# Performance work log

Measured on AMD Instinct MI355X. Metric: run time of the kernel, lower is better.

## Reference

```python
import jax, jax.numpy as jnp
import numpy as np

B, N, K, IN_CH = 512, 64, 16, 6   # graphs, nodes per graph, knn, input features
EPS = 1e-5


def _w(key, shape, fan_in):
    return jax.random.normal(key, shape, jnp.float32) / np.sqrt(fan_in)


def setup_inputs() -> dict:
    key = jax.random.key(0)
    ks = jax.random.split(key, 16)
    f32 = jnp.float32
    inp = {
        "x": jax.random.normal(ks[0], (B * N, IN_CH), f32),
        "batch": (jnp.arange(B * N, dtype=jnp.int32) // N).astype(jnp.int32),
        # input projection 6 -> 64
        "w_in": _w(ks[1], (IN_CH, 64), IN_CH), "g_in": jnp.ones(64, f32), "b_in": jnp.zeros(64, f32),
        # ec1: SharedMLP([128, 64, 64])
        "w1a": _w(ks[2], (128, 64), 128), "g1a": jnp.ones(64, f32), "b1a": jnp.zeros(64, f32),
        "w1b": _w(ks[3], (64, 64), 64),   "g1b": jnp.ones(64, f32), "b1b": jnp.zeros(64, f32),
        # ec2: SharedMLP([128, 128, 128])
        "w2a": _w(ks[4], (128, 128), 128), "g2a": jnp.ones(128, f32), "b2a": jnp.zeros(128, f32),
        "w2b": _w(ks[5], (128, 128), 128), "g2b": jnp.ones(128, f32), "b2b": jnp.zeros(128, f32),
        # ec3: SharedMLP([256, 256, 256])
        "w3a": _w(ks[6], (256, 256), 256), "g3a": jnp.ones(256, f32), "b3a": jnp.zeros(256, f32),
        "w3b": _w(ks[7], (256, 256), 256), "g3b": jnp.ones(256, f32), "b3b": jnp.zeros(256, f32),
        # classifier head (dropout is identity in eval mode)
        "wc1": _w(ks[8], (896, 512), 896), "gc1": jnp.ones(512, f32), "bc1": jnp.zeros(512, f32),
        "wc2": _w(ks[9], (512, 256), 512), "gc2": jnp.ones(256, f32), "bc2": jnp.zeros(256, f32),
        "wc3": _w(ks[10], (256, 2), 256),  "bc3": jnp.zeros(2, f32),
    }
    return inp


def bn(h, g, b):
    # training-mode BatchNorm1d over all leading (node/edge) dims, biased var
    ax = tuple(range(h.ndim - 1))
    m = h.mean(ax)
    v = h.var(ax)
    return g * (h - m) * jax.lax.rsqrt(v + EPS) + b


def lrelu(h):
    return jax.nn.leaky_relu(h, 0.2)


def knn(x):
    # x: [B,N,C]; per-graph squared-Euclidean kNN (excluding self)
    sq = jnp.sum(x * x, -1)
    d = sq[:, :, None] - 2.0 * jnp.einsum('bnc,bmc->bnm', x, x) + sq[:, None, :]
    _, idx = jax.lax.top_k(-d, K + 1)  # K+1 smallest distances
    return idx[:, :, 1:]               # drop self -> [B,N,K]


def edge_conv(x, w1, g1, b1, w2, g2, b2):
    # Dynamic EdgeConv, aggr='max'. Edge (src=centre c, dst=neighbour n):
    # target x_i = x_n, message = MLP(cat[x_i, x_j - x_i]) with x_j = x_c.
    idx = knn(x)                                     # [B,N,K]
    xn = jax.vmap(lambda xb, ib: xb[ib])(x, idx)     # [B,N,K,C] neighbours
    xc = x[:, :, None, :]                            # centres broadcast
    feat = jnp.concatenate([xn, xc - xn], -1)        # [B,N,K,2C]
    h = lrelu(bn(feat @ w1, g1, b1))
    h = lrelu(bn(h @ w2, g2, b2))                    # [B,N,K,Cout]
    C = h.shape[-1]

    def scatter_max(ib, hb):  # per-graph max-scatter to destination nodes
        out = jnp.full((N, C), -jnp.inf, hb.dtype)
        return out.at[ib.reshape(-1)].max(hb.reshape(-1, C))

    res = jax.vmap(scatter_max)(idx, h)
    return jnp.where(jnp.isneginf(res), 0.0, res)    # nodes w/o in-edges -> 0


def reference(x, batch, w_in, g_in, b_in,
              w1a, g1a, b1a, w1b, g1b, b1b,
              w2a, g2a, b2a, w2b, g2b, b2b,
              w3a, g3a, b3a, w3b, g3b, b3b,
              wc1, gc1, bc1, wc2, gc2, bc2, wc3, bc3):
    # batch == arange(B*N)//N (equal-size graphs), encoded by the [B,N] reshape
    h0 = lrelu(bn(x @ w_in, g_in, b_in)).reshape(B, N, 64)
    h1 = edge_conv(h0, w1a, g1a, b1a, w1b, g1b, b1b)   # [B,N,64]
    h2 = edge_conv(h1, w2a, g2a, b2a, w2b, g2b, b2b)   # [B,N,128]
    h3 = edge_conv(h2, w3a, g3a, b3a, w3b, g3b, b3b)   # [B,N,256]
    h = jnp.concatenate([h1, h2, h3], -1)              # [B,N,448]
    pooled = jnp.concatenate([h.mean(1), h.max(1)], -1)  # [B,896]
    z = lrelu(bn(pooled @ wc1, gc1, bc1))
    z = lrelu(bn(z @ wc2, gc2, bc2))
    return z @ wc3 + bc3                               # [B,2] logits
```

## Files before the change

kernel.cpp:

```cpp
#include <hip/hip_runtime.h>
#include <hip/hip_fp16.h>
#include <math.h>

#define BB 512
#define NN 64
#define KNB 16
#define NPTS (BB*NN)
#define NEDGE (BB*NN*KNB)
#define EPSV 1e-5f

typedef __attribute__((ext_vector_type(8))) _Float16 f16x8;
typedef __attribute__((ext_vector_type(4))) _Float16 f16x4;
typedef __attribute__((ext_vector_type(4))) float f32x4;

__device__ __forceinline__ float lrelu(float x){ return x > 0.0f ? x : 0.2f*x; }
__device__ __forceinline__ unsigned encf(float f){
    unsigned u = __float_as_uint(f);
    return (u & 0x80000000u) ? ~u : (u | 0x80000000u);
}
__device__ __forceinline__ float decf(unsigned e){
    unsigned u = (e & 0x80000000u) ? (e ^ 0x80000000u) : ~e;
    return __uint_as_float(u);
}
#define ENC_NEGINF 0x007FFFFFu

__device__ __forceinline__ void split2h(float v, _Float16& h, _Float16& m){
    h = (_Float16)v;
    float r = v - (float)h;
    m = (_Float16)(r * 2048.0f);
}

__global__ void k_input(const float* __restrict__ x, const float* __restrict__ w,
                        float* __restrict__ h0){
    __shared__ float wls[6*64];
    int t = threadIdx.x;
    for (int i = t; i < 6*64; i += 256) wls[i] = w[i];
    __syncthreads();
    int row = blockIdx.x*256 + t;
    float xv[6];
#pragma unroll
    for (int k = 0; k < 6; k++) xv[k] = x[row*6 + k];
#pragma unroll 8
    for (int c = 0; c < 64; c++){
        float acc = 0.f;
#pragma unroll
        for (int k = 0; k < 6; k++) acc += xv[k]*wls[k*64 + c];
        h0[(size_t)row*64 + c] = acc;
    }
}

__global__ void k_colstats_part(const float* __restrict__ h,
                                float* __restrict__ pS, float* __restrict__ pQ){
    int t = threadIdx.x;
    int c = t & 63;
    int g = t >> 6;
    int p = blockIdx.x*4 + g;
    const int rpb = NPTS/256;
    int r0 = p*rpb;
    float s = 0.f, q = 0.f;
    for (int r = r0; r < r0 + rpb; r++){
        float v = h[(size_t)r*64 + c];
        s += v; q += v*v;
    }
    pS[c*256 + p] = s;
    pQ[c*256 + p] = q;
}

__global__ void k_bnfin_part(const float* __restrict__ pS, const float* __restrict__ pQ,
                             const float* __restrict__ g, const float* __restrict__ b,
                             float* __restrict__ cA, float* __restrict__ cB,
                             int P, float invM){
    int c = threadIdx.x;
    const float* ps = pS + (size_t)c*P;
    const float* pq = pQ + (size_t)c*P;
    float s = 0.f, q = 0.f;
    for (int p = 0; p < P; p += 4){
        float4 vs = *(const float4*)(ps + p);
        float4 vq = *(const float4*)(pq + p);
        s += vs.x + vs.y + vs.z + vs.w;
        q += vq.x + vq.y + vq.z + vq.w;
    }
    float m = s*invM;
    float v = q*invM - m*m;
    v = v < 0.f ? 0.f : v;
    float a = g[c]*rsqrtf(v + EPSV);
    cA[c] = a;
    cB[c] = b[c] - m*a;
}

__global__ void k_bnfin(const float* gs, const float* gq, const float* g,
                        const float* b, float* cA, float* cB, int C, float invM){
    int c = blockIdx.x*blockDim.x + threadIdx.x;
    if (c < C){
        float m = gs[c]*invM;
        float v = gq[c]*invM - m*m;
        v = v < 0.f ? 0.f : v;
        float a = g[c]*rsqrtf(v + EPSV);
        cA[c] = a;
        cB[c] = b[c] - m*a;
    }
}

__global__ void k_apply(float* h, const float* __restrict__ cA,
                        const float* __restrict__ cB, int C, int total){
    int i = blockIdx.x*256 + threadIdx.x;
    if (i < total){
        int c = i & (C-1);
        h[i] = lrelu(cA[c]*h[i] + cB[c]);
    }
}

template<int C>
__global__ void k_knn(const float* __restrict__ x, int* __restrict__ idxg){
    const int CP = C + 4;
    __shared__ __align__(16) float xls[64*CP];
    __shared__ float sq[64];
    __shared__ __align__(16) float dls[64*64];
    int t = threadIdx.x, b = blockIdx.x;
    const float* xb = x + (size_t)b*64*C;
    for (int i = t; i < 64*C; i += 256){
        int n = i / C, c = i & (C-1);
        xls[n*CP + c] = xb[i];
    }
    __syncthreads();
    if (t < 64){
        float s = 0.f;
        for (int c = 0; c < C; c += 4){
            float4 v = *(const float4*)&xls[t*CP + c];
            s += v.x*v.x + v.y*v.y + v.z*v.z + v.w*v.w;
        }
        sq[t] = s;
    }
    __syncthreads();
    {
        int n  = t >> 2;
        int m0 = (t & 3)*16;
        float acc[16];
#pragma unroll
        for (int i = 0; i < 16; i++) acc[i] = 0.f;
        const float* an = &xls[n*CP];
        const float* bm = &xls[m0*CP];
        for (int c = 0; c < C; c += 4){
            float4 a = *(const float4*)(an + c);
#pragma unroll
            for (int i = 0; i < 16; i++){
                float4 bv = *(const float4*)(bm + i*CP + c);
                acc[i] += a.x*bv.x + a.y*bv.y + a.z*bv.z + a.w*bv.w;
            }
        }
        float sn = sq[n];
#pragma unroll
        for (int i4 = 0; i4 < 16; i4 += 4){
            float4 dv;
            dv.x = sn - 2.0f*acc[i4+0] + sq[m0+i4+0];
            dv.y = sn - 2.0f*acc[i4+1] + sq[m0+i4+1];
            dv.z = sn - 2.0f*acc[i4+2] + sq[m0+i4+2];
            dv.w = sn - 2.0f*acc[i4+3] + sq[m0+i4+3];
            *(float4*)&dls[n*64 + m0 + i4] = dv;
        }
    }
    __syncthreads();
    int lane = t & 63, w = t >> 6;
    for (int pr = 0; pr < 16; pr += 4){
        int n0 = w*16 + pr;
        unsigned long long c0 = (((unsigned long long)encf(dls[(n0+0)*64 + lane])) << 32) | (unsigned)lane;
        unsigned long long c1 = (((unsigned long long)encf(dls[(n0+1)*64 + lane])) << 32) | (unsigned)lane;
        unsigned long long c2 = (((unsigned long long)encf(dls[(n0+2)*64 + lane])) << 32) | (unsigned)lane;
        unsigned long long c3 = (((unsigned long long)encf(dls[(n0+3)*64 + lane])) << 32) | (unsigned)lane;
#pragma unroll
        for (int k = 2; k <= 64; k <<= 1){
#pragma unroll
            for (int j = k >> 1; j > 0; j >>= 1){
                bool keepmin = ((lane & j) == 0) == ((lane & k) == 0);
                unsigned long long o0 = __shfl_xor(c0, j, 64);
                unsigned long long o1 = __shfl_xor(c1, j, 64);
                unsigned long long o2 = __shfl_xor(c2, j, 64);
                unsigned long long o3 = __shfl_xor(c3, j, 64);
                c0 = keepmin ? (c0 < o0 ? c0 : o0) : (c0 < o0 ? o0 : c0);
                c1 = keepmin ? (c1 < o1 ? c1 : o1) : (c1 < o1 ? o1 : c1);
                c2 = keepmin ? (c2 < o2 ? c2 : o2) : (c2 < o2 ? o2 : c2);
                c3 = keepmin ? (c3 < o3 ? c3 : o3) : (c3 < o3 ? o3 : c3);
            }
        }
        if (lane >= 1 && lane <= KNB){
            int base = b*1024 + n0*16 + lane - 1;
            idxg[base]      = (int)(c0 & 0xffffffffu);
            idxg[base + 16] = (int)(c1 & 0xffffffffu);
            idxg[base + 32] = (int)(c2 & 0xffffffffu);
            idxg[base + 48] = (int)(c3 & 0xffffffffu);
        }
    }
}

template<int CIN, int CMID, bool SPLIT>
__global__ void k_wprep(const float* __restrict__ w1,
                        _Float16* __restrict__ wbh, _Float16* __restrict__ wbm,
                        _Float16* __restrict__ wdh, _Float16* __restrict__ wdm){
    int i = blockIdx.x*256 + threadIdx.x;
    if (i >= CIN*CMID) return;
    int k = i / CMID, c = i - k*CMID;
    float wb = w1[(size_t)(CIN + k)*CMID + c];
    float wd = w1[(size_t)k*CMID + c] - wb;
    size_t o = (size_t)c*CIN + k;
    if (SPLIT){
        _Float16 h, m;
        split2h(wb, h, m); wbh[o] = h; wbm[o] = m;
        split2h(wd, h, m); wdh[o] = h; wdm[o] = m;
    } else {
        wbh[o] = (_Float16)wb;
        wdh[o] = (_Float16)wd;
    }
}

template<int CIN, int CMID>
__global__ __launch_bounds__(256)
void k_mm1x(const float* __restrict__ x,
            const _Float16* __restrict__ wbh, const _Float16* __restrict__ wbm,
            const _Float16* __restrict__ wdh, const _Float16* __restrict__ wdm,
            float* __restrict__ P, float* __restrict__ Q){
    int t = threadIdx.x, b = blockIdx.x;
    int lane = t & 63, w = t >> 6;
    int lrow = lane & 15, lk = lane >> 4;
    const int KT = CIN/32;
    f16x8 ah[KT], am[KT];
    {
        const float* xr = x + ((size_t)b*64 + w*16 + lrow)*CIN;
#pragma unroll
        for (int kt = 0; kt < KT; kt++){
            union { f16x8 v; _Float16 u[8]; } H, M;
#pragma unroll
            for (int j = 0; j < 8; j++)
                split2h(xr[kt*32 + lk*8 + j], H.u[j], M.u[j]);
            ah[kt] = H.v; am[kt] = M.v;
        }
    }
#pragma unroll
    for (int ct = 0; ct < CMID/16; ct++){
        int col = ct*16 + lrow;
        f32x4 aPM = {0,0,0,0}, aPC = {0,0,0,0};
        f32x4 aQM = {0,0,0,0}, aQC = {0,0,0,0};
#pragma unroll
        for (int kt = 0; kt < KT; kt++){
            size_t bo = (size_t)col*CIN + kt*32 + lk*8;
            f16x8 bbh = *(const f16x8*)(wbh + bo);
            f16x8 bbm = *(const f16x8*)(wbm + bo);
            f16x8 bdh = *(const f16x8*)(wdh + bo);
            f16x8 bdm = *(const f16x8*)(wdm + bo);
            aPM = __builtin_amdgcn_mfma_f32_16x16x32_f16(ah[kt], bbh, aPM, 0, 0, 0);
            aPC = __builtin_amdgcn_mfma_f32_16x16x32_f16(ah[kt], bbm, aPC, 0, 0, 0);
            aPC = __builtin_amdgcn_mfma_f32_16x16x32_f16(am[kt], bbh, aPC, 0, 0, 0);
            aQM = __builtin_amdgcn_mfma_f32_16x16x32_f16(ah[kt], bdh, aQM, 0, 0, 0);
            aQC = __builtin_amdgcn_mfma_f32_16x16x32_f16(ah[kt], bdm, aQC, 0, 0, 0);
            aQC = __builtin_amdgcn_mfma_f32_16x16x32_f16(am[kt], bdh, aQC, 0, 0, 0);
        }
#pragma unroll
        for (int u = 0; u < 4; u++){
            size_t o = ((size_t)b*64 + w*16 + lk*4 + u)*CMID + col;
            P[o] = aPM[u] + aPC[u]*(1.0f/2048.0f);
            Q[o] = aQM[u] + aQC[u]*(1.0f/2048.0f);
        }
    }
}

template<int CIN, int CMID>
__global__ __launch_bounds__(256)
void k_mm1xh(const float* __restrict__ x,
             const _Float16* __restrict__ wbh, const _Float16* __restrict__ wdh,
             _Float16* __restrict__ P, _Float16* __restrict__ Q){
    int t = threadIdx.x, b = blockIdx.x;
    int lane = t & 63, w = t >> 6;
    int lrow = lane & 15, lk = lane >> 4;
    const int KT = CIN/32;
    f16x8 ah[KT];
    {
        const float* xr = x + ((size_t)b*64 + w*16 + lrow)*CIN;
#pragma unroll
        for (int kt = 0; kt < KT; kt++){
            union { f16x8 v; _Float16 u[8]; } H;
#pragma unroll
            for (int j = 0; j < 8; j++)
                H.u[j] = (_Float16)xr[kt*32 + lk*8 + j];
            ah[kt] = H.v;
        }
    }
#pragma unroll
    for (int ct = 0; ct < CMID/16; ct++){
        int col = ct*16 + lrow;
        f32x4 aP = {0,0,0,0}, aQ = {0,0,0,0};
#pragma unroll
        for (int kt = 0; kt < KT; kt++){
            size_t bo = (size_t)col*CIN + kt*32 + lk*8;
            f16x8 bbh = *(const f16x8*)(wbh + bo);
            f16x8 bdh = *(const f16x8*)(wdh + bo);
            aP = __builtin_amdgcn_mfma_f32_16x16x32_f16(ah[kt], bbh, aP, 0, 0, 0);
            aQ = __builtin_amdgcn_mfma_f32_16x16x32_f16(ah[kt], bdh, aQ, 0, 0, 0);
        }
#pragma unroll
        for (int u = 0; u < 4; u++){
            size_t o = ((size_t)b*64 + w*16 + lk*4 + u)*CMID + col;
            P[o] = (_Float16)aP[u];
            Q[o] = (_Float16)aQ[u];
        }
    }
}

template<int CMID>
__global__ void k_stats1p(const float* __restrict__ P, const float* __restrict__ Q,
                          const int* __restrict__ idxg,
                          float* __restrict__ pS, float* __restrict__ pQ){
    int t = threadIdx.x, b = blockIdx.x;
    const int NG = 256/CMID;
    const int PT = 512*NG;
    int c = t & (CMID-1);
    int g = t / CMID;
    int epg = 1024/NG;
    const float* Pb = P + (size_t)b*64*CMID;
    const float* Qb = Q + (size_t)b*64*CMID;
    const int* ib = idxg + b*1024;
    float s = 0.f, q = 0.f;
    for (int e = g*epg; e < (g+1)*epg; e++){
        int n = e >> 4;
        int j = ib[e];
        float v = Pb[n*CMID + c] + Qb[j*CMID + c];
        s += v; q += v*v;
    }
    int p = b*NG + g;
    pS[(size_t)c*PT + p] = s;
    pQ[(size_t)c*PT + p] = q;
}

__global__ void k_stats1h(const _Float16* __restrict__ P, const _Float16* __restrict__ Q,
                          const int* __restrict__ idxg,
                          float* __restrict__ pS, float* __restrict__ pQ){
    __shared__ int ils[1024];
    int t = threadIdx.x, b = blockIdx.x;
    for (int i = t; i < 1024; i += 256) ils[i] = idxg[b*1024 + i];
    __syncthreads();
    const _Float16* Pb = P + (size_t)b*64*256;
    const _Float16* Qb = Q + (size_t)b*64*256;
    float s = 0.f, q = 0.f;
    for (int n = 0; n < 64; n++){
        float p = (float)Pb[n*256 + t];
#pragma unroll 4
        for (int k = 0; k < 16; k++){
            int j = ils[n*16 + k];
            float v = p + (float)Qb[j*256 + t];
            s += v; q += v*v;
        }
    }
    pS[(size_t)t*512 + b] = s;
    pQ[(size_t)t*512 + b] = q;
}

template<int CMID, int COUT, int NSET>
__global__ __launch_bounds__(256, 3)
void k_mm2s(const float* __restrict__ P, const float* __restrict__ Q,
            const int* __restrict__ idxg,
            const float* __restrict__ cA1, const float* __restrict__ cB1,
            const float* __restrict__ w2, const float* __restrict__ g2,
            unsigned* __restrict__ outenc,
            float* __restrict__ pS, float* __restrict__ pQ){
    const int AS = CMID + 8;
    const int NCOL = 64*NSET;
    __shared__ __align__(16) _Float16 act_h[32*AS];
    __shared__ __align__(16) _Float16 act_m[32*AS];
    __shared__ unsigned maxtab[NCOL*64];
    __shared__ unsigned short ils[1024];
    __shared__ __align__(16) float a1ls[CMID];
    __shared__ __align__(16) float b1ls[CMID];
    int t = threadIdx.x, b = blockIdx.x, cc = blockIdx.y;
    int lane = t & 63, w = t >> 6;
    int lrow = lane & 15, lk = lane >> 4;

    for (int i = t; i < 1024; i += 256) ils[i] = (unsigned short)idxg[b*1024 + i];
    for (int i = t; i < CMID; i += 256){ a1ls[i] = cA1[i]; b1ls[i] = cB1[i]; }
    for (int i = t; i < NCOL*64; i += 256) maxtab[i] = ENC_NEGINF;

    const int KT = CMID/32;
    f16x8 bh[NSET][KT], bm[NSET][KT];
    float sg[NSET];
    int ccBase = cc*NCOL;
#pragma unroll
    for (int s = 0; s < NSET; s++){
        int ncol = ccBase + s*64 + w*16 + lrow;
#pragma unroll
        for (int kt = 0; kt < KT; kt++){
            union { f16x8 v; _Float16 u[8]; } uh, um;
#pragma unroll
            for (int j = 0; j < 8; j++){
                int k = kt*32 + lk*8 + j;
                split2h(w2[(size_t)k*COUT + ncol], uh.u[j], um.u[j]);
            }
            bh[s][kt] = uh.v; bm[s][kt] = um.v;
        }
        sg[s] = (g2[ncol] < 0.0f) ? -1.0f : 1.0f;
    }
    float ss[NSET], qq[NSET];
#pragma unroll
    for (int s = 0; s < NSET; s++){ ss[s] = 0.f; qq[s] = 0.f; }
    const float* Pb = P + (size_t)b*64*CMID;
    const float* Qb = Q + (size_t)b*64*CMID;
    __syncthreads();

    for (int ch = 0; ch < 32; ch++){
        for (int i = t*4; i < 32*CMID; i += 1024){
            int le = i / CMID, k = i & (CMID-1);
            int e = ch*32 + le;
            int n = e >> 4, j = ils[e];
            float4 pv = *(const float4*)(Pb + n*CMID + k);
            float4 qv = *(const float4*)(Qb + j*CMID + k);
            float4 ca = *(const float4*)&a1ls[k];
            float4 cb = *(const float4*)&b1ls[k];
            float v0 = lrelu(ca.x*(pv.x + qv.x) + cb.x);
            float v1 = lrelu(ca.y*(pv.y + qv.y) + cb.y);
            float v2 = lrelu(ca.z*(pv.z + qv.z) + cb.z);
            float v3 = lrelu(ca.w*(pv.w + qv.w) + cb.w);
            union { f16x4 v; _Float16 u[4]; } hh, mm;
            split2h(v0, hh.u[0], mm.u[0]);
            split2h(v1, hh.u[1], mm.u[1]);
            split2h(v2, hh.u[2], mm.u[2]);
            split2h(v3, hh.u[3], mm.u[3]);
            *(f16x4*)&act_h[le*AS + k] = hh.v;
            *(f16x4*)&act_m[le*AS + k] = mm.v;
        }
        __syncthreads();

        f32x4 accM[2][NSET], accC[2][NSET];
#pragma unroll
        for (int r = 0; r < 2; r++)
#pragma unroll
            for (int s = 0; s < NSET; s++){
                accM[r][s] = {0.f,0.f,0.f,0.f};
                accC[r][s] = {0.f,0.f,0.f,0.f};
            }
#pragma unroll
        for (int kt = 0; kt < KT; kt++){
            int ko = kt*32 + lk*8;
#pragma unroll
            for (int r = 0; r < 2; r++){
                f16x8 ah = *(const f16x8*)&act_h[(r*16 + lrow)*AS + ko];
                f16x8 am = *(const f16x8*)&act_m[(r*16 + lrow)*AS + ko];
#pragma unroll
                for (int s = 0; s < NSET; s++){
                    accM[r][s] = __builtin_amdgcn_mfma_f32_16x16x32_f16(ah, bh[s][kt], accM[r][s], 0, 0, 0);
                    accC[r][s] = __builtin_amdgcn_mfma_f32_16x16x32_f16(ah, bm[s][kt], accC[r][s], 0, 0, 0);
                    accC[r][s] = __builtin_amdgcn_mfma_f32_16x16x32_f16(am, bh[s][kt], accC[r][s], 0, 0, 0);
                }
            }
        }
#pragma unroll
        for (int r = 0; r < 2; r++){
#pragma unroll
            for (int s = 0; s < NSET; s++){
                int colL = s*64 + w*16 + lrow;
#pragma unroll
                for (int u = 0; u < 4; u++){
                    int e = ch*32 + r*16 + lk*4 + u;
                    float v = accM[r][s][u] + accC[r][s][u]*(1.0f/2048.0f);
                    ss[s] += v; qq[s] += v*v;
                    int j = ils[e];
                    atomicMax(&maxtab[colL*64 + (j ^ (colL & 31))], encf(sg[s]*v));
                }
            }
        }
        __syncthreads();
    }
#pragma unroll
    for (int s = 0; s < NSET; s++){
        ss[s] += __shfl_xor(ss[s], 16, 64); ss[s] += __shfl_xor(ss[s], 32, 64);
        qq[s] += __shfl_xor(qq[s], 16, 64); qq[s] += __shfl_xor(qq[s], 32, 64);
        if (lane < 16){
            pS[(size_t)(ccBase + s*64 + w*16 + lane)*512 + b] = ss[s];
            pQ[(size_t)(ccBase + s*64 + w*16 + lane)*512 + b] = qq[s];
        }
    }
    for (int i = t; i < 64*NCOL; i += 256){
        int colL = i % NCOL, j = i / NCOL;
        outenc[((size_t)b*64 + j)*COUT + ccBase + colL] = maxtab[colL*64 + (j ^ (colL & 31))];
    }
}

template<int CMID, int COUT, int NSET>
__global__ __launch_bounds__(256, 3)
void k_mm2xh(const _Float16* __restrict__ P, const _Float16* __restrict__ Q,
             const int* __restrict__ idxg,
             const float* __restrict__ cA1, const float* __restrict__ cB1,
             const float* __restrict__ w2, const float* __restrict__ g2,
             unsigned* __restrict__ outenc,
             float* __restrict__ pS, float* __restrict__ pQ){
    const int AS = CMID + 8;
    const int NCOL = 64*NSET;
    __shared__ __align__(16) _Float16 act[32*AS];
    __shared__ unsigned maxtab[NCOL*64];
    __shared__ unsigned short ils[1024];
    __shared__ __align__(16) _Float16 a1h[CMID];
    __shared__ __align__(16) _Float16 b1h[CMID];
    int t = threadIdx.x, b = blockIdx.x, cc = blockIdx.y;
    int lane = t & 63, w = t >> 6;
    int lrow = lane & 15, lk = lane >> 4;

    for (int i = t; i < 1024; i += 256) ils[i] = (unsigned short)idxg[b*1024 + i];
    for (int i = t; i < CMID; i += 256){
        a1h[i] = (_Float16)cA1[i];
        b1h[i] = (_Float16)cB1[i];
    }
    for (int i = t; i < NCOL*64; i += 256) maxtab[i] = ENC_NEGINF;

    const int KT = CMID/32;
    f16x8 breg[NSET][KT];
    float sg[NSET];
    int ccBase = cc*NCOL;
#pragma unroll
    for (int s = 0; s < NSET; s++){
        int ncol = ccBase + s*64 + w*16 + lrow;
#pragma unroll
        for (int kt = 0; kt < KT; kt++){
            union { f16x8 v; _Float16 u[8]; } bu;
#pragma unroll
            for (int j = 0; j < 8; j++){
                int k = kt*32 + lk*8 + j;
                bu.u[j] = (_Float16)w2[(size_t)k*COUT + ncol];
            }
            breg[s][kt] = bu.v;
        }
        sg[s] = (g2[ncol] < 0.0f) ? -1.0f : 1.0f;
    }
    float ss[NSET], qq[NSET];
#pragma unroll
    for (int s = 0; s < NSET; s++){ ss[s] = 0.f; qq[s] = 0.f; }
    const _Float16* Pb = P + (size_t)b*64*CMID;
    const _Float16* Qb = Q + (size_t)b*64*CMID;
    __syncthreads();

    for (int ch = 0; ch < 32; ch++){
        for (int i = t*8; i < 32*CMID; i += 2048){
            int le = i / CMID, k = i & (CMID-1);
            int e = ch*32 + le;
            int n = e >> 4, j = ils[e];
            f16x8 pv = *(const f16x8*)(Pb + (size_t)n*CMID + k);
            f16x8 qv = *(const f16x8*)(Qb + (size_t)j*CMID + k);
            f16x8 ca = *(const f16x8*)&a1h[k];
            f16x8 cb = *(const f16x8*)&b1h[k];
            f16x8 v = ca*(pv + qv) + cb;
            f16x8 vm = v * (_Float16)0.2f;
            union { f16x8 x; _Float16 e8[8]; } V, M, R;
            V.x = v; M.x = vm;
#pragma unroll
            for (int u = 0; u < 8; u++)
                R.e8[u] = (V.e8[u] > (_Float16)0.0f) ? V.e8[u] : M.e8[u];
            *(f16x8*)&act[le*AS + k] = R.x;
        }
        __syncthreads();

        f32x4 acc[2][NSET];
#pragma unroll
        for (int r = 0; r < 2; r++)
#pragma unroll
            for (int s = 0; s < NSET; s++) acc[r][s] = {0.f,0.f,0.f,0.f};
#pragma unroll
        for (int kt = 0; kt < KT; kt++){
            int ko = kt*32 + lk*8;
#pragma unroll
            for (int r = 0; r < 2; r++){
                f16x8 a = *(const f16x8*)&act[(r*16 + lrow)*AS + ko];
#pragma unroll
                for (int s = 0; s < NSET; s++)
                    acc[r][s] = __builtin_amdgcn_mfma_f32_16x16x32_f16(a, breg[s][kt], acc[r][s], 0, 0, 0);
            }
        }
#pragma unroll
        for (int r = 0; r < 2; r++){
#pragma unroll
            for (int s = 0; s < NSET; s++){
                int colL = s*64 + w*16 + lrow;
#pragma unroll
                for (int u = 0; u < 4; u++){
                    int e = ch*32 + r*16 + lk*4 + u;
                    float v = acc[r][s][u];
                    ss[s] += v; qq[s] += v*v;
                    int j = ils[e];
                    atomicMax(&maxtab[colL*64 + (j ^ (colL & 31))], encf(sg[s]*v));
                }
            }
        }
        __syncthreads();
    }
#pragma unroll
    for (int s = 0; s < NSET; s++){
        ss[s] += __shfl_xor(ss[s], 16, 64); ss[s] += __shfl_xor(ss[s], 32, 64);
        qq[s] += __shfl_xor(qq[s], 16, 64); qq[s] += __shfl_xor(qq[s], 32, 64);
        if (lane < 16){
            pS[(size_t)(ccBase + s*64 + w*16 + lane)*512 + b] = ss[s];
            pQ[(size_t)(ccBase + s*64 + w*16 + lane)*512 + b] = qq[s];
        }
    }
    for (int i = t; i < 64*NCOL; i += 256){
        int colL = i % NCOL, j = i / NCOL;
        outenc[((size_t)b*64 + j)*COUT + ccBase + colL] = maxtab[colL*64 + (j ^ (colL & 31))];
    }
}

__global__ void k_final_ec(unsigned* __restrict__ buf, const float* __restrict__ cA,
                           const float* __restrict__ cB, const float* __restrict__ g,
                           int C, int total){
    int i = blockIdx.x*256 + threadIdx.x;
    if (i >= total) return;
    int c = i & (C-1);
    unsigned e = buf[i];
    float r;
    if (e == ENC_NEGINF) r = 0.0f;
    else {
        float s = (g[c] < 0.0f) ? -1.0f : 1.0f;
        float v = s*decf(e);
        r = lrelu(cA[c]*v + cB[c]);
    }
    ((float*)buf)[i] = r;
}

__global__ void k_pool(const float* __restrict__ h1, const float* __restrict__ h2,
                       const float* __restrict__ h3, float* __restrict__ pooled){
    int t = threadIdx.x, b = blockIdx.x;
    for (int c = t; c < 448; c += 256){
        const float* src; int C, cl;
        if (c < 64){ src = h1; C = 64;  cl = c; }
        else if (c < 192){ src = h2; C = 128; cl = c - 64; }
        else { src = h3; C = 256; cl = c - 192; }
        const float* p = src + (size_t)b*64*C + cl;
        float s = 0.f, mx = -INFINITY;
        for (int n = 0; n < 64; n++){
            float v = p[(size_t)n*C];
            s += v; mx = fmaxf(mx, v);
        }
        pooled[b*896 + c] = s*(1.0f/64.0f);
        pooled[b*896 + 448 + c] = mx;
    }
}

__global__ void k_fc1(const float* __restrict__ pooled, const float* __restrict__ w,
                      float* __restrict__ z, float* gs, float* gq){
    int r = blockIdx.x;
    int co = blockIdx.y*256 + threadIdx.x;
    const float* pr = pooled + r*896;
    float acc = 0.f;
    for (int k = 0; k < 896; k++) acc += pr[k]*w[(size_t)k*512 + co];
    z[(size_t)r*512 + co] = acc;
    atomicAdd(&gs[co], acc);
    atomicAdd(&gq[co], acc*acc);
}

__global__ void k_fc2(const float* __restrict__ z1, const float* __restrict__ cA,
                      const float* __restrict__ cB, const float* __restrict__ w,
                      float* __restrict__ z2, float* gs, float* gq){
    int r = blockIdx.x;
    int co = threadIdx.x;
    const float* zr = z1 + (size_t)r*512;
    float acc = 0.f;
    for (int k = 0; k < 512; k++){
        float v = lrelu(cA[k]*zr[k] + cB[k]);
        acc += v*w[(size_t)k*256 + co];
    }
    z2[(size_t)r*256 + co] = acc;
    atomicAdd(&gs[co], acc);
    atomicAdd(&gq[co], acc*acc);
}

__global__ void k_fc3(const float* __restrict__ z2, const float* __restrict__ cA,
                      const float* __restrict__ cB, const float* __restrict__ w,
                      const float* __restrict__ bias, float* __restrict__ out){
    int r = blockIdx.x*256 + threadIdx.x;
    const float* zr = z2 + (size_t)r*256;
    float a0 = 0.f, a1 = 0.f;
    for (int k = 0; k < 256; k++){
        float v = lrelu(cA[k]*zr[k] + cB[k]);
        a0 += v*w[k*2 + 0];
        a1 += v*w[k*2 + 1];
    }
    out[r*2 + 0] = a0 + bias[0];
    out[r*2 + 1] = a1 + bias[1];
}

extern "C" void kernel_launch(void* const* d_in, const int* in_sizes, int n_in,
                              void* d_out, int out_size, void* d_ws, size_t ws_size,
                              hipStream_t stream){
    const float* x    = (const float*)d_in[0];
    const float* w_in = (const float*)d_in[2];
    const float* g_in = (const float*)d_in[3];
    const float* b_in = (const float*)d_in[4];
    const float* w1a  = (const float*)d_in[5];
    const float* g1a  = (const float*)d_in[6];
    const float* b1a  = (const float*)d_in[7];
    const float* w1b  = (const float*)d_in[8];
    const float* g1b  = (const float*)d_in[9];
    const float* b1b  = (const float*)d_in[10];
    const float* w2a  = (const float*)d_in[11];
    const float* g2a  = (const float*)d_in[12];
    const float* b2a  = (const float*)d_in[13];
    const float* w2b  = (const float*)d_in[14];
    const float* g2b  = (const float*)d_in[15];
    const float* b2b  = (const float*)d_in[16];
    const float* w3a  = (const float*)d_in[17];
    const float* g3a  = (const float*)d_in[18];
    const float* b3a  = (const float*)d_in[19];
    const float* w3b  = (const float*)d_in[20];
    const float* g3b  = (const float*)d_in[21];
    const float* b3b  = (const float*)d_in[22];
    const float* wc1  = (const float*)d_in[23];
    const float* gc1  = (const float*)d_in[24];
    const float* bc1  = (const float*)d_in[25];
    const float* wc2  = (const float*)d_in[26];
    const float* gc2  = (const float*)d_in[27];
    const float* bc2  = (const float*)d_in[28];
    const float* wc3  = (const float*)d_in[29];
    const float* bc3  = (const float*)d_in[30];

    char* ws = (char*)d_ws;
    size_t off = 0;
    auto alloc = [&](size_t bytes){
        size_t o = off; off = (off + bytes + 255) & ~(size_t)255; return o;
    };
    float* h0     = (float*)(ws + alloc((size_t)NPTS*64*4));
    float* h1     = (float*)(ws + alloc((size_t)NPTS*64*4));
    float* h2     = (float*)(ws + alloc((size_t)NPTS*128*4));
    float* h3     = (float*)(ws + alloc((size_t)NPTS*256*4));
    float* P      = (float*)(ws + alloc((size_t)NPTS*256*4));
    float* Q      = (float*)(ws + alloc((size_t)NPTS*256*4));
    int*   idx    = (int*)  (ws + alloc((size_t)NPTS*16*4));
    float* pooled = (float*)(ws + alloc((size_t)512*896*4));
    float* z1     = (float*)(ws + alloc((size_t)512*512*4));
    float* z2     = (float*)(ws + alloc((size_t)512*256*4));
    float* pS     = (float*)(ws + alloc((size_t)131072*4));
    float* pQ     = (float*)(ws + alloc((size_t)131072*4));
    float* stats  = (float*)(ws + alloc((size_t)2048*4));
    float* coefs  = (float*)(ws + alloc((size_t)3456*4));
    _Float16* wsp = (_Float16*)(ws + alloc((size_t)114688*2));

    _Float16 *w1bh = wsp,          *w1bm = wsp+4096,
             *w1dh = wsp+8192,     *w1dm = wsp+12288;
    _Float16 *w2bh = wsp+16384,    *w2bm = wsp+24576,
             *w2dh = wsp+32768,    *w2dm = wsp+40960;
    _Float16 *w3bh = wsp+49152,    *w3dh = wsp+81920;

    float *f1s  = stats,       *f1q  = stats+512;
    float *f2s  = stats+1024,  *f2q  = stats+1280;
    float *cA0   = coefs,      *cB0   = coefs+64;
    float *cA1a  = coefs+128,  *cB1a  = coefs+192;
    float *cA1b  = coefs+256,  *cB1b  = coefs+320;
    float *cA2a  = coefs+384,  *cB2a  = coefs+512;
    float *cA2b  = coefs+640,  *cB2b  = coefs+768;
    float *cA3a  = coefs+896,  *cB3a  = coefs+1152;
    float *cA3b  = coefs+1408, *cB3b  = coefs+1664;
    float *cAf1  = coefs+1920, *cBf1  = coefs+2432;
    float *cAf2  = coefs+2944, *cBf2  = coefs+3200;

    (void)hipMemsetAsync(stats, 0, 2048*4, stream);

    k_wprep<64,64,true><<<16, 256, 0, stream>>>(w1a, w1bh, w1bm, w1dh, w1dm);
    k_wprep<64,128,true><<<32, 256, 0, stream>>>(w2a, w2bh, w2bm, w2dh, w2dm);
    k_wprep<128,256,false><<<128, 256, 0, stream>>>(w3a, w3bh, nullptr, w3dh, nullptr);

    k_input<<<NPTS/256, 256, 0, stream>>>(x, w_in, h0);
    k_colstats_part<<<64, 256, 0, stream>>>(h0, pS, pQ);
    k_bnfin_part<<<1, 64, 0, stream>>>(pS, pQ, g_in, b_in, cA0, cB0, 256, 1.0f/NPTS);
    k_apply<<<(NPTS*64)/256, 256, 0, stream>>>(h0, cA0, cB0, 64, NPTS*64);

    k_knn<64><<<BB, 256, 0, stream>>>(h0, idx);
    k_mm1x<64,64><<<BB, 256, 0, stream>>>(h0, w1bh, w1bm, w1dh, w1dm, P, Q);
    k_stats1p<64><<<BB, 256, 0, stream>>>(P, Q, idx, pS, pQ);
    k_bnfin_part<<<1, 64, 0, stream>>>(pS, pQ, g1a, b1a, cA1a, cB1a, 2048, 1.0f/NEDGE);
    k_mm2s<64,64,1><<<dim3(BB,1), 256, 0, stream>>>(P, Q, idx, cA1a, cB1a, w1b, g1b,
                                                    (unsigned*)h1, pS, pQ);
    k_bnfin_part<<<1, 64, 0, stream>>>(pS, pQ, g1b, b1b, cA1b, cB1b, 512, 1.0f/NEDGE);
    k_final_ec<<<(NPTS*64)/256, 256, 0, stream>>>((unsigned*)h1, cA1b, cB1b, g1b, 64, NPTS*64);

    k_knn<64><<<BB, 256, 0, stream>>>(h1, idx);
    k_mm1x<64,128><<<BB, 256, 0, stream>>>(h1, w2bh, w2bm, w2dh, w2dm, P, Q);
    k_stats1p<128><<<BB, 256, 0, stream>>>(P, Q, idx, pS, pQ);
    k_bnfin_part<<<1, 128, 0, stream>>>(pS, pQ, g2a, b2a, cA2a, cB2a, 1024, 1.0f/NEDGE);
    k_mm2s<128,128,2><<<dim3(BB,1), 256, 0, stream>>>(P, Q, idx, cA2a, cB2a, w2b, g2b,
                                                      (unsigned*)h2, pS, pQ);
    k_bnfin_part<<<1, 128, 0, stream>>>(pS, pQ, g2b, b2b, cA2b, cB2b, 512, 1.0f/NEDGE);
    k_final_ec<<<(NPTS*128)/256, 256, 0, stream>>>((unsigned*)h2, cA2b, cB2b, g2b, 128, NPTS*128);

    k_knn<128><<<BB, 256, 0, stream>>>(h2, idx);
    k_mm1xh<128,256><<<BB, 256, 0, stream>>>(h2, w3bh, w3dh, (_Float16*)P, (_Float16*)Q);
    k_stats1h<<<BB, 256, 0, stream>>>((_Float16*)P, (_Float16*)Q, idx, pS, pQ);
    k_bnfin_part<<<1, 256, 0, stream>>>(pS, pQ, g3a, b3a, cA3a, cB3a, 512, 1.0f/NEDGE);
    k_mm2xh<256,256,2><<<dim3(BB,2), 256, 0, stream>>>((_Float16*)P, (_Float16*)Q, idx,
                                                       cA3a, cB3a, w3b, g3b,
                                                       (unsigned*)h3, pS, pQ);
    k_bnfin_part<<<1, 256, 0, stream>>>(pS, pQ, g3b, b3b, cA3b, cB3b, 512, 1.0f/NEDGE);
    k_final_ec<<<(NPTS*256)/256, 256, 0, stream>>>((unsigned*)h3, cA3b, cB3b, g3b, 256, NPTS*256);

    k_pool<<<BB, 256, 0, stream>>>(h1, h2, h3, pooled);
    k_fc1<<<dim3(512,2), 256, 0, stream>>>(pooled, wc1, z1, f1s, f1q);
    k_bnfin<<<2, 256, 0, stream>>>(f1s, f1q, gc1, bc1, cAf1, cBf1, 512, 1.0f/512);
    k_fc2<<<512, 256, 0, stream>>>(z1, cAf1, cBf1, wc2, z2, f2s, f2q);
    k_bnfin<<<1, 256, 0, stream>>>(f2s, f2q, gc2, bc2, cAf2, cBf2, 256, 1.0f/512);
    k_fc3<<<2, 256, 0, stream>>>(z2, cAf2, cBf2, wc3, bc3, (float*)d_out);

    (void)in_sizes; (void)n_in; (void)out_size; (void)ws_size;
}
```

Measured before the change: 1.238 ms.

## Fold BN affine into P/Q and build MFMA operands directly from global

Adds a small elementwise kernel that pre-applies the layer-3a BatchNorm scale and shift to the fp16 P and Q buffers. The k_mm2xh kernel can then build each A fragment in registers straight from global P/Q rows, skipping the shared-memory activation staging and two barriers per chunk. The launch-bounds occupancy hint is also removed. The cost is an extra pass over P and Q. Each wave now issues redundant scattered global loads, since the fragments are no longer shared through LDS.

```diff
diff --git a/kernel.cpp b/kernel.cpp
--- a/kernel.cpp
+++ b/kernel.cpp
@@ -108,6 +108,19 @@
         int c = i & (C-1);
         h[i] = lrelu(cA[c]*h[i] + cB[c]);
     }
+}
+
+__global__ void k_pqfold(_Float16* __restrict__ P, _Float16* __restrict__ Q,
+                         const float* __restrict__ cA, const float* __restrict__ cB){
+    int i = (blockIdx.x*256 + threadIdx.x)*8;
+    int k = i & 255;
+    f16x8 ca, cb;
+#pragma unroll
+    for (int u = 0; u < 8; u++){ ca[u] = (_Float16)cA[k+u]; cb[u] = (_Float16)cB[k+u]; }
+    f16x8 p = *(const f16x8*)(P + i);
+    f16x8 q = *(const f16x8*)(Q + i);
+    *(f16x8*)(P + i) = ca*p + cb;
+    *(f16x8*)(Q + i) = ca*q;
 }
 
 template<int C>
@@ -481,29 +494,20 @@
 }
 
 template<int CMID, int COUT, int NSET>
-__global__ __launch_bounds__(256, 3)
+__global__ __launch_bounds__(256)
 void k_mm2xh(const _Float16* __restrict__ P, const _Float16* __restrict__ Q,
              const int* __restrict__ idxg,
-             const float* __restrict__ cA1, const float* __restrict__ cB1,
              const float* __restrict__ w2, const float* __restrict__ g2,
              unsigned* __restrict__ outenc,
              float* __restrict__ pS, float* __restrict__ pQ){
-    const int AS = CMID + 8;
     const int NCOL = 64*NSET;
-    __shared__ __align__(16) _Float16 act[32*AS];
     __shared__ unsigned maxtab[NCOL*64];
     __shared__ unsigned short ils[1024];
-    __shared__ __align__(16) _Float16 a1h[CMID];
-    __shared__ __align__(16) _Float16 b1h[CMID];
     int t = threadIdx.x, b = blockIdx.x, cc = blockIdx.y;
     int lane = t & 63, w = t >> 6;
     int lrow = lane & 15, lk = lane >> 4;
 
     for (int i = t; i < 1024; i += 256) ils[i] = (unsigned short)idxg[b*1024 + i];
-    for (int i = t; i < CMID; i += 256){
-        a1h[i] = (_Float16)cA1[i];
-        b1h[i] = (_Float16)cB1[i];
-    }
     for (int i = t; i < NCOL*64; i += 256) maxtab[i] = ENC_NEGINF;
 
     const int KT = CMID/32;
@@ -533,39 +537,32 @@
     __syncthreads();
 
     for (int ch = 0; ch < 32; ch++){
-        for (int i = t*8; i < 32*CMID; i += 2048){
-            int le = i / CMID, k = i & (CMID-1);
-            int e = ch*32 + le;
-            int n = e >> 4, j = ils[e];
-            f16x8 pv = *(const f16x8*)(Pb + (size_t)n*CMID + k);
-            f16x8 qv = *(const f16x8*)(Qb + (size_t)j*CMID + k);
-            f16x8 ca = *(const f16x8*)&a1h[k];
-            f16x8 cb = *(const f16x8*)&b1h[k];
-            f16x8 v = ca*(pv + qv) + cb;
-            f16x8 vm = v * (_Float16)0.2f;
-            union { f16x8 x; _Float16 e8[8]; } V, M, R;
-            V.x = v; M.x = vm;
-#pragma unroll
-            for (int u = 0; u < 8; u++)
-                R.e8[u] = (V.e8[u] > (_Float16)0.0f) ? V.e8[u] : M.e8[u];
-            *(f16x8*)&act[le*AS + k] = R.x;
-        }
-        __syncthreads();
-
         f32x4 acc[2][NSET];
 #pragma unroll
         for (int r = 0; r < 2; r++)
 #pragma unroll
             for (int s = 0; s < NSET; s++) acc[r][s] = {0.f,0.f,0.f,0.f};
 #pragma unroll
-        for (int kt = 0; kt < KT; kt++){
-            int ko = kt*32 + lk*8;
-#pragma unroll
-            for (int r = 0; r < 2; r++){
-                f16x8 a = *(const f16x8*)&act[(r*16 + lrow)*AS + ko];
+        for (int r = 0; r < 2; r++){
+            int n = ch*2 + r;
+            int j = ils[ch*32 + r*16 + lrow];
+            const _Float16* Pr = Pb + (size_t)n*CMID;
+            const _Float16* Qr = Qb + (size_t)j*CMID;
+#pragma unroll
+            for (int kt = 0; kt < KT; kt++){
+                int ko = kt*32 + lk*8;
+                f16x8 p = *(const f16x8*)(Pr + ko);
+                f16x8 q = *(const f16x8*)(Qr + ko);
+                f16x8 v = p + q;
+                f16x8 vm = v * (_Float16)0.2f;
+                union { f16x8 x; _Float16 e8[8]; } V, M, R;
+                V.x = v; M.x = vm;
+#pragma unroll
+                for (int u = 0; u < 8; u++)
+                    R.e8[u] = (V.e8[u] > (_Float16)0.0f) ? V.e8[u] : M.e8[u];
 #pragma unroll
                 for (int s = 0; s < NSET; s++)
-                    acc[r][s] = __builtin_amdgcn_mfma_f32_16x16x32_f16(a, breg[s][kt], acc[r][s], 0, 0, 0);
+                    acc[r][s] = __builtin_amdgcn_mfma_f32_16x16x32_f16(R.x, breg[s][kt], acc[r][s], 0, 0, 0);
             }
         }
 #pragma unroll
@@ -583,8 +580,8 @@
                 }
             }
         }
-        __syncthreads();
-    }
+    }
+    __syncthreads();
 #pragma unroll
     for (int s = 0; s < NSET; s++){
         ss[s] += __shfl_xor(ss[s], 16, 64); ss[s] += __shfl_xor(ss[s], 32, 64);
@@ -785,9 +782,9 @@
     k_mm1xh<128,256><<<BB, 256, 0, stream>>>(h2, w3bh, w3dh, (_Float16*)P, (_Float16*)Q);
     k_stats1h<<<BB, 256, 0, stream>>>((_Float16*)P, (_Float16*)Q, idx, pS, pQ);
     k_bnfin_part<<<1, 256, 0, stream>>>(pS, pQ, g3a, b3a, cA3a, cB3a, 512, 1.0f/NEDGE);
+    k_pqfold<<<(NPTS*256)/(256*8), 256, 0, stream>>>((_Float16*)P, (_Float16*)Q, cA3a, cB3a);
     k_mm2xh<256,256,2><<<dim3(BB,2), 256, 0, stream>>>((_Float16*)P, (_Float16*)Q, idx,
-                                                       cA3a, cB3a, w3b, g3b,
-                                                       (unsigned*)h3, pS, pQ);
+                                                       w3b, g3b, (unsigned*)h3, pS, pQ);
     k_bnfin_part<<<1, 256, 0, stream>>>(pS, pQ, g3b, b3b, cA3b, cB3b, 512, 1.0f/NEDGE);
     k_final_ec<<<(NPTS*256)/256, 256, 0, stream>>>((unsigned*)h3, cA3b, cB3b, g3b, 256, NPTS*256);
 
```

Result: slower. 1.459 ms (+17.8%).
